# Performance work log

Measured on AMD Instinct MI355X. Metric: run time of the kernel, lower is better.

## Reference

```python
import jax, jax.numpy as jnp
import numpy as np


def setup_inputs() -> dict:
    key = jax.random.key(0)
    k1, k2, k3, k4 = jax.random.split(key, 4)
    B, C_in, C_out, H, W = 8, 256, 256, 160, 160
    mask = jax.random.randint(k1, (B, 1, H, W), 0, 2, dtype=jnp.int32)  # binary hard mask
    ori = jax.random.normal(k2, (B, C_in, H, W), dtype=jnp.float32)
    weight = jax.random.normal(k3, (C_out, C_in, 3, 3), dtype=jnp.float32) * 0.02
    bias = jax.random.normal(k4, (C_out,), dtype=jnp.float32) * 0.02
    return {"mask": mask, "ori": ori, "weight": weight, "bias": bias}


def reference(mask, ori, weight, bias):
    # apply_mask: broadcast binary [B,1,H,W] mask over channels, zero masked regions
    x = ori * mask.astype(ori.dtype)
    # dense 3x3 conv, stride 1, padding 1 (SAME) -> output [B, C_out, H, W]
    out = jax.lax.conv_general_dilated(
        x, weight,
        window_strides=(1, 1),
        padding='SAME',
        dimension_numbers=('NCHW', 'OIHW', 'NCHW'),
    )
    return out + bias[None, :, None, None]
```

## Files before the change

kernel.cpp:

```cpp
#include <hip/hip_runtime.h>

typedef __attribute__((ext_vector_type(8))) short short8;
typedef __attribute__((ext_vector_type(4))) float f32x4;

#define B_    8
#define CI    256
#define CO    256
#define Hh    160
#define Ww    160
#define HP    162
#define WP    162
#define HWp   (Hh * Ww)
#define XPAD_ELEMS (B_ * HP * WP * CI)
#define W3_ELEMS   (9 * CI * CO)
#define NT    36
#define BSLOT 8192

__device__ __forceinline__ unsigned short f2bf(float f) {
  unsigned int u = __float_as_uint(f);
  u += 0x7FFFu + ((u >> 16) & 1u);
  return (unsigned short)(u >> 16);
}

__global__ void prep_w_kernel(const float* __restrict__ w, unsigned short* __restrict__ w3) {
  int i = blockIdx.x * 256 + threadIdx.x;
  if (i >= W3_ELEMS) return;
  int e = i & 7, l = (i >> 3) & 63, g = i >> 9;
  int mi = g & 1, wm = (g >> 1) & 3, kk = (g >> 3) & 1;
  int qm = (g >> 4) & 1, cic = (g >> 5) & 3, shift = g >> 7;
  int co = qm * 128 + wm * 32 + mi * 16 + (l & 15);
  int ci = cic * 64 + kk * 32 + (l >> 4) * 8 + e;
  w3[i] = f2bf(w[(co * 256 + ci) * 9 + shift]);
}

__global__ void zero_border(unsigned short* __restrict__ xp) {
  int g = blockIdx.x * 256 + threadIdx.x;
  int pos = g >> 5;
  int c = (g & 31) << 3;
  int n = pos / 644;
  int p = pos - n * 644;
  int y, x;
  if (p < 324) { y = (p < 162) ? 0 : 161; x = (p < 162) ? p : p - 162; }
  else { int q = p - 324; y = 1 + (q >> 1); x = (q & 1) ? 161 : 0; }
  unsigned short* d = xp + (((size_t)(n * 162 + y)) * 162 + x) * 256 + c;
  *(uint4*)d = (uint4){0u, 0u, 0u, 0u};
}

__global__ void prep_x_kernel(const float* __restrict__ ori, const int* __restrict__ mask,
                              unsigned short* __restrict__ xp) {
  int bid = blockIdx.x;
  int wt = bid % 3;
  int t1 = bid / 3;
  int cit = t1 & 3;
  int t2 = t1 >> 2;
  int h = t2 % Hh;
  int n = t2 / Hh;
  int t = threadIdx.x;

  __shared__ float tile[64][65];

  int wl = t & 63;
  int w = wt * 64 + wl;
  bool valid = (w < Ww);
  float m = 0.f;
  if (valid) m = (float)mask[(n * Hh + h) * Ww + w];
  const float* src = ori + (((size_t)(n * CI + cit * 64) * Hh + h) * Ww + w);
  int r0 = t >> 6;
#pragma unroll
  for (int k = 0; k < 16; ++k) {
    int ci_l = r0 * 16 + k;
    float v = 0.f;
    if (valid) v = src[(size_t)ci_l * HWp] * m;
    tile[ci_l][wl] = v;
  }
  __syncthreads();

  int wl2 = t >> 2;
  int wo = wt * 64 + wl2;
  if (wo < Ww) {
    int cseg = (t & 3) * 16;
    union { unsigned short u[8]; uint4 v; } p0, p1;
#pragma unroll
    for (int j = 0; j < 8; ++j) p0.u[j] = f2bf(tile[cseg + j][wl2]);
#pragma unroll
    for (int j = 0; j < 8; ++j) p1.u[j] = f2bf(tile[cseg + 8 + j][wl2]);
    unsigned short* dst = xp + ((size_t)((n * HP + h + 1) * WP) + (wo + 1)) * CI + cit * 64 + cseg;
    *(uint4*)dst = p0.v;
    *(uint4*)(dst + 8) = p1.v;
  }
}

__device__ __forceinline__ void gload16(const unsigned short* g, unsigned short* l) {
  __builtin_amdgcn_global_load_lds((const __attribute__((address_space(1))) void*)g,
                                   (__attribute__((address_space(3))) void*)l, 16, 0, 0);
}

__global__ void __launch_bounds__(256, 2)
sconv_gemm(const unsigned short* __restrict__ xp, const unsigned short* __restrict__ w3,
           const float* __restrict__ bias, float* __restrict__ out) {
  __shared__ unsigned short Bs[3][BSLOT];

  const int bid = blockIdx.x;
  const int n = bid & 7;
  const int pxt = bid >> 3;
  const int p0 = pxt * 128;

  const int t = threadIdx.x;
  const int l = t & 63;
  const int wv = t >> 6;

  const int lr = l >> 3;
  const int swz8 = ((l & 7) ^ lr) << 3;
  const int lc = l & 15, hi4 = l >> 4, lx7 = l & 7;

  unsigned boff[4];
#pragma unroll
  for (int g = 0; g < 4; ++g) {
    int p = p0 + wv * 32 + g * 8 + lr;
    int h = p / Ww;
    int w = p - h * Ww;
    boff[g] = (unsigned)((n * HP + h) * WP + w) * 256 + swz8;
  }

  f32x4 acc[2][2][8];
#pragma unroll
  for (int a = 0; a < 2; ++a)
#pragma unroll
    for (int b = 0; b < 2; ++b)
#pragma unroll
      for (int c = 0; c < 8; ++c)
        acc[a][b][c] = (f32x4){0.f, 0.f, 0.f, 0.f};

  auto STAGE = [&](int ts, unsigned short* slot) {
    int cic = (ts * 57) >> 9;
    int sh = ts - cic * 9;
    int kh = (sh * 11) >> 5;
    int kw = sh - kh * 3;
    const unsigned short* src = xp + (unsigned)(kh * WP + kw) * 256 + (cic << 6);
    unsigned short* dst = slot + wv * 2048;
#pragma unroll
    for (int g = 0; g < 4; ++g)
      gload16(src + boff[g], dst + g * 512);
  };

  auto AG = [&](int ts, short8* a) {
    int cic = (ts * 57) >> 9;
    int sh = ts - cic * 9;
    const unsigned short* p = w3 + (((unsigned)(sh * 128 + cic * 32 + wv * 2)) << 9) + (l << 3);
    a[0] = *(const short8*)(p);
    a[1] = *(const short8*)(p + 512);
    a[2] = *(const short8*)(p + 4096);
    a[3] = *(const short8*)(p + 4096 + 512);
    a[4] = *(const short8*)(p + 8192);
    a[5] = *(const short8*)(p + 8192 + 512);
    a[6] = *(const short8*)(p + 8192 + 4096);
    a[7] = *(const short8*)(p + 8192 + 4096 + 512);
  };

#define BBL4(dst, slot, kk, nb) do {                                          \
  _Pragma("unroll")                                                           \
  for (int ni = 0; ni < 4; ++ni)                                              \
    dst[ni] = *(const short8*)((slot) + (((nb) + ni) * 16 + lc) * 64 +        \
                               (((((kk) << 2) + hi4) ^ lx7) << 3));           \
} while (0)

#define CL16(A, kk, bb, nb) do {                                              \
  __builtin_amdgcn_s_setprio(1);                                              \
  _Pragma("unroll")                                                           \
  for (int qm = 0; qm < 2; ++qm)                                              \
    _Pragma("unroll")                                                         \
    for (int mi = 0; mi < 2; ++mi)                                            \
      _Pragma("unroll")                                                       \
      for (int ni = 0; ni < 4; ++ni)                                          \
        acc[qm][mi][(nb) + ni] = __builtin_amdgcn_mfma_f32_16x16x32_bf16(     \
            A[qm * 4 + (kk) * 2 + mi], bb[ni], acc[qm][mi][(nb) + ni], 0, 0, 0); \
  __builtin_amdgcn_s_setprio(0);                                              \
} while (0)

  short8 aA[8], bbA[4], bbB[4];

#define TILE(tt, cur, sdst, WN) do {                                          \
  AG((tt), aA);                                    \
  if ((tt) + 2 < NT) STAGE((tt) + 2, (sdst));                                 \
  BBL4(bbA, (cur), 0, 0);                                                     \
  BBL4(bbB, (cur), 0, 4);                                                     \
  CL16(aA, 0, bbA, 0);                                                        \
  BBL4(bbA, (cur), 1, 0);                                                     \
  CL16(aA, 0, bbB, 4);                                                        \
  BBL4(bbB, (cur), 1, 4);                                                     \
  CL16(aA, 1, bbA, 0);                                                        \
  CL16(aA, 1, bbB, 4);                                                        \
  asm volatile("s_waitcnt vmcnt(" #WN ")" ::: "memory");                      \
  __builtin_amdgcn_s_barrier();                                               \
} while (0)

  unsigned short* const s0 = &Bs[0][0];
  unsigned short* const s1 = &Bs[1][0];
  unsigned short* const s2 = &Bs[2][0];

  STAGE(0, s0);
  STAGE(1, s1);
  asm volatile("s_waitcnt vmcnt(4)" ::: "memory");
  __builtin_amdgcn_s_barrier();

  for (int t3 = 0; t3 < 33; t3 += 3) {
    TILE(t3 + 0, s0, s2, 4);
    TILE(t3 + 1, s1, s0, 4);
    TILE(t3 + 2, s2, s1, 4);
  }
  TILE(33, s0, s2, 4);
  TILE(34, s1, s0, 0);
  {
    AG(35, aA);
    BBL4(bbA, s2, 0, 0);
    BBL4(bbB, s2, 0, 4);
    CL16(aA, 0, bbA, 0);
    BBL4(bbA, s2, 1, 0);
    CL16(aA, 0, bbB, 4);
    BBL4(bbB, s2, 1, 4);
    CL16(aA, 1, bbA, 0);
    CL16(aA, 1, bbB, 4);
  }

#pragma unroll
  for (int qm = 0; qm < 2; ++qm)
#pragma unroll
    for (int mi = 0; mi < 2; ++mi) {
      int cobase = qm * 128 + wv * 32 + mi * 16 + hi4 * 4;
      const float4 bv = *(const float4*)(bias + cobase);
#pragma unroll
      for (int ni = 0; ni < 8; ++ni) {
        int p = p0 + ni * 16 + lc;
        float* op = out + ((size_t)n * CO + cobase) * HWp + p;
        f32x4 v = acc[qm][mi][ni];
        op[0]               = v[0] + bv.x;
        op[(size_t)HWp]     = v[1] + bv.y;
        op[(size_t)2 * HWp] = v[2] + bv.z;
        op[(size_t)3 * HWp] = v[3] + bv.w;
      }
    }
}

extern "C" void kernel_launch(void* const* d_in, const int* in_sizes, int n_in,
                              void* d_out, int out_size, void* d_ws, size_t ws_size,
                              hipStream_t stream) {
  const int* mask = (const int*)d_in[0];
  const float* ori = (const float*)d_in[1];
  const float* weight = (const float*)d_in[2];
  const float* bias = (const float*)d_in[3];
  float* out = (float*)d_out;

  unsigned short* xp = (unsigned short*)d_ws;
  unsigned short* w3 = xp + XPAD_ELEMS;

  zero_border<<<644, 256, 0, stream>>>(xp);
  prep_w_kernel<<<(W3_ELEMS + 255) / 256, 256, 0, stream>>>(weight, w3);
  prep_x_kernel<<<B_ * Hh * 4 * 3, 256, 0, stream>>>(ori, mask, xp);
  sconv_gemm<<<1600, 256, 0, stream>>>(xp, w3, bias, out);
}
```

Before: 337.1 us.

## Retile implicit-GEMM conv to one output row per block with split-K phases

Each block now computes a full 160-pixel output row for all 256 output channels, with each wave owning 64 output channels across 10 pixel subtiles, replacing the 128-pixel by 256-channel tiles. Each tile's K step is split into four barrier-separated phases. Input staging is spread across those phases and weight fragments for the next tile are prefetched in halves. The aim is to cut per-row index math, reuse staged input across more MFMAs, and overlap global loads with compute. In exchange it uses more barriers, a larger LDS slot, 1280 blocks instead of 1600, and more accumulator registers that may lower occupancy.

```diff
diff --git a/kernel.cpp b/kernel.cpp
--- a/kernel.cpp
+++ b/kernel.cpp
@@ -14,7 +14,7 @@
 #define XPAD_ELEMS (B_ * HP * WP * CI)
 #define W3_ELEMS   (9 * CI * CO)
 #define NT    36
-#define BSLOT 8192
+#define BSLOT (160 * 64)
 
 __device__ __forceinline__ unsigned short f2bf(float f) {
   unsigned int u = __float_as_uint(f);
@@ -102,8 +102,7 @@
 
   const int bid = blockIdx.x;
   const int n = bid & 7;
-  const int pxt = bid >> 3;
-  const int p0 = pxt * 128;
+  const int h = bid >> 3;
 
   const int t = threadIdx.x;
   const int l = t & 63;
@@ -112,133 +111,131 @@
   const int lr = l >> 3;
   const int swz8 = ((l & 7) ^ lr) << 3;
   const int lc = l & 15, hi4 = l >> 4, lx7 = l & 7;
-
-  unsigned boff[4];
-#pragma unroll
-  for (int g = 0; g < 4; ++g) {
-    int p = p0 + wv * 32 + g * 8 + lr;
-    int h = p / Ww;
-    int w = p - h * Ww;
-    boff[g] = (unsigned)((n * HP + h) * WP + w) * 256 + swz8;
-  }
-
-  f32x4 acc[2][2][8];
-#pragma unroll
-  for (int a = 0; a < 2; ++a)
-#pragma unroll
-    for (int b = 0; b < 2; ++b)
-#pragma unroll
-      for (int c = 0; c < 8; ++c)
-        acc[a][b][c] = (f32x4){0.f, 0.f, 0.f, 0.f};
-
-  auto STAGE = [&](int ts, unsigned short* slot) {
-    int cic = (ts * 57) >> 9;
-    int sh = ts - cic * 9;
-    int kh = (sh * 11) >> 5;
-    int kw = sh - kh * 3;
-    const unsigned short* src = xp + (unsigned)(kh * WP + kw) * 256 + (cic << 6);
-    unsigned short* dst = slot + wv * 2048;
-#pragma unroll
-    for (int g = 0; g < 4; ++g)
-      gload16(src + boff[g], dst + g * 512);
+  const unsigned xrow = (unsigned)(n * HP + h);
+
+  unsigned boff[5];
+#pragma unroll
+  for (int k = 0; k < 5; ++k)
+    boff[k] = (unsigned)(k * 32 + wv * 8 + lr) * 256 + swz8;
+
+  f32x4 acc[4][10];
+#pragma unroll
+  for (int j = 0; j < 4; ++j)
+#pragma unroll
+    for (int ni = 0; ni < 10; ++ni)
+      acc[j][ni] = (f32x4){0.f, 0.f, 0.f, 0.f};
+
+  short8 aK0[4], aK1[4], bb[5];
+
+#define TPAR(ts, cic, sh, kh, kw)                                             \
+  const int cic = ((ts) * 57) >> 9;                                           \
+  const int sh = (ts) - cic * 9;                                              \
+  const int kh = (sh * 11) >> 5;                                              \
+  const int kw = sh - kh * 3;
+
+  auto STG = [&](int ts, unsigned short* slot, int k) {
+    TPAR(ts, cic, sh, kh, kw)
+    (void)sh;
+    const unsigned short* src = xp + ((size_t)(xrow + kh) * WP + kw) * 256 + (cic << 6) + boff[k];
+    gload16(src, slot + (k * 32 + wv * 8) * 64);
   };
 
-  auto AG = [&](int ts, short8* a) {
-    int cic = (ts * 57) >> 9;
-    int sh = ts - cic * 9;
-    const unsigned short* p = w3 + (((unsigned)(sh * 128 + cic * 32 + wv * 2)) << 9) + (l << 3);
-    a[0] = *(const short8*)(p);
-    a[1] = *(const short8*)(p + 512);
-    a[2] = *(const short8*)(p + 4096);
-    a[3] = *(const short8*)(p + 4096 + 512);
-    a[4] = *(const short8*)(p + 8192);
-    a[5] = *(const short8*)(p + 8192 + 512);
-    a[6] = *(const short8*)(p + 8192 + 4096);
-    a[7] = *(const short8*)(p + 8192 + 4096 + 512);
+  auto AGH = [&](int ts, int kk, short8* dst) {
+    TPAR(ts, cic, sh, kh, kw)
+    (void)kh; (void)kw;
+    const unsigned short* p = w3 +
+        ((size_t)(sh * 128 + cic * 32 + (wv >> 1) * 16 + ((wv & 1) << 2) + kk * 8) << 9) + (l << 3);
+#pragma unroll
+    for (int j = 0; j < 4; ++j)
+      dst[j] = *(const short8*)(p + (j << 9));
   };
 
-#define BBL4(dst, slot, kk, nb) do {                                          \
+#define BBR(slot, kk, nb) do {                                                \
   _Pragma("unroll")                                                           \
-  for (int ni = 0; ni < 4; ++ni)                                              \
-    dst[ni] = *(const short8*)((slot) + (((nb) + ni) * 16 + lc) * 64 +        \
-                               (((((kk) << 2) + hi4) ^ lx7) << 3));           \
-} while (0)
-
-#define CL16(A, kk, bb, nb) do {                                              \
+  for (int i = 0; i < 5; ++i)                                                 \
+    bb[i] = *(const short8*)((slot) + (((nb) + i) * 16 + lc) * 64 +           \
+                             (((((kk) << 2) + hi4) ^ lx7) << 3));             \
+} while (0)
+
+#define CL(AH, nb) do {                                                       \
   __builtin_amdgcn_s_setprio(1);                                              \
   _Pragma("unroll")                                                           \
-  for (int qm = 0; qm < 2; ++qm)                                              \
+  for (int j = 0; j < 4; ++j)                                                 \
     _Pragma("unroll")                                                         \
-    for (int mi = 0; mi < 2; ++mi)                                            \
-      _Pragma("unroll")                                                       \
-      for (int ni = 0; ni < 4; ++ni)                                          \
-        acc[qm][mi][(nb) + ni] = __builtin_amdgcn_mfma_f32_16x16x32_bf16(     \
-            A[qm * 4 + (kk) * 2 + mi], bb[ni], acc[qm][mi][(nb) + ni], 0, 0, 0); \
+    for (int i = 0; i < 5; ++i)                                               \
+      acc[j][(nb) + i] = __builtin_amdgcn_mfma_f32_16x16x32_bf16(             \
+          AH[j], bb[i], acc[j][(nb) + i], 0, 0, 0);                           \
   __builtin_amdgcn_s_setprio(0);                                              \
 } while (0)
 
-  short8 aA[8], bbA[4], bbB[4];
-
-#define TILE(tt, cur, sdst, WN) do {                                          \
-  AG((tt), aA);                                    \
-  if ((tt) + 2 < NT) STAGE((tt) + 2, (sdst));                                 \
-  BBL4(bbA, (cur), 0, 0);                                                     \
-  BBL4(bbB, (cur), 0, 4);                                                     \
-  CL16(aA, 0, bbA, 0);                                                        \
-  BBL4(bbA, (cur), 1, 0);                                                     \
-  CL16(aA, 0, bbB, 4);                                                        \
-  BBL4(bbB, (cur), 1, 4);                                                     \
-  CL16(aA, 1, bbA, 0);                                                        \
-  CL16(aA, 1, bbB, 4);                                                        \
-  asm volatile("s_waitcnt vmcnt(" #WN ")" ::: "memory");                      \
+#define PH(slot, kk, AH, nb, ISSUES, ENDW) do {                               \
+  ISSUES                                                                      \
+  BBR(slot, kk, nb);                                                          \
   __builtin_amdgcn_s_barrier();                                               \
+  asm volatile("s_waitcnt lgkmcnt(0)" ::: "memory");                          \
+  __builtin_amdgcn_sched_barrier(0);                                          \
+  CL(AH, nb);                                                                 \
+  ENDW                                                                        \
+  __builtin_amdgcn_s_barrier();                                               \
+} while (0)
+
+#define TILE(tt, sc, sn) do {                                                 \
+  PH(sc, 0, aK0, 0, { STG((tt) + 2, sn, 0); STG((tt) + 2, sn, 1); }, {});     \
+  PH(sc, 0, aK0, 5, { STG((tt) + 2, sn, 2); }, {});                           \
+  PH(sc, 1, aK1, 0, { AGH((tt) + 1, 0, aK0); STG((tt) + 2, sn, 3); }, {});    \
+  PH(sc, 1, aK1, 5, { STG((tt) + 2, sn, 4); },                                \
+     { AGH((tt) + 1, 1, aK1);                                                 \
+       asm volatile("s_waitcnt vmcnt(13)" ::: "memory"); });                  \
 } while (0)
 
   unsigned short* const s0 = &Bs[0][0];
   unsigned short* const s1 = &Bs[1][0];
   unsigned short* const s2 = &Bs[2][0];
 
-  STAGE(0, s0);
-  STAGE(1, s1);
-  asm volatile("s_waitcnt vmcnt(4)" ::: "memory");
+  for (int k = 0; k < 5; ++k) STG(0, s0, k);
+  for (int k = 0; k < 5; ++k) STG(1, s1, k);
+  AGH(0, 0, aK0);
+  AGH(0, 1, aK1);
+  asm volatile("s_waitcnt vmcnt(13)" ::: "memory");
   __builtin_amdgcn_s_barrier();
 
   for (int t3 = 0; t3 < 33; t3 += 3) {
-    TILE(t3 + 0, s0, s2, 4);
-    TILE(t3 + 1, s1, s0, 4);
-    TILE(t3 + 2, s2, s1, 4);
-  }
-  TILE(33, s0, s2, 4);
-  TILE(34, s1, s0, 0);
+    TILE(t3 + 0, s0, s2);
+    TILE(t3 + 1, s1, s0);
+    TILE(t3 + 2, s2, s1);
+  }
+  TILE(33, s0, s2);
+  PH(s1, 0, aK0, 0, {}, {});
+  PH(s1, 0, aK0, 5, {}, {});
+  PH(s1, 1, aK1, 0, { AGH(35, 0, aK0); }, {});
+  PH(s1, 1, aK1, 5, {},
+     { AGH(35, 1, aK1);
+       asm volatile("s_waitcnt vmcnt(8)" ::: "memory"); });
+  PH(s2, 0, aK0, 0, {}, {});
+  PH(s2, 0, aK0, 5, {}, {});
+  PH(s2, 1, aK1, 0, {}, {});
   {
-    AG(35, aA);
-    BBL4(bbA, s2, 0, 0);
-    BBL4(bbB, s2, 0, 4);
-    CL16(aA, 0, bbA, 0);
-    BBL4(bbA, s2, 1, 0);
-    CL16(aA, 0, bbB, 4);
-    BBL4(bbB, s2, 1, 4);
-    CL16(aA, 1, bbA, 0);
-    CL16(aA, 1, bbB, 4);
-  }
-
-#pragma unroll
-  for (int qm = 0; qm < 2; ++qm)
-#pragma unroll
-    for (int mi = 0; mi < 2; ++mi) {
-      int cobase = qm * 128 + wv * 32 + mi * 16 + hi4 * 4;
-      const float4 bv = *(const float4*)(bias + cobase);
-#pragma unroll
-      for (int ni = 0; ni < 8; ++ni) {
-        int p = p0 + ni * 16 + lc;
-        float* op = out + ((size_t)n * CO + cobase) * HWp + p;
-        f32x4 v = acc[qm][mi][ni];
-        op[0]               = v[0] + bv.x;
-        op[(size_t)HWp]     = v[1] + bv.y;
-        op[(size_t)2 * HWp] = v[2] + bv.z;
-        op[(size_t)3 * HWp] = v[3] + bv.w;
-      }
+    BBR(s2, 1, 5);
+    asm volatile("s_waitcnt lgkmcnt(0)" ::: "memory");
+    __builtin_amdgcn_sched_barrier(0);
+    CL(aK1, 5);
+  }
+
+#pragma unroll
+  for (int j = 0; j < 4; ++j) {
+    int cobase = wv * 64 + j * 16 + hi4 * 4;
+    const float4 bv = *(const float4*)(bias + cobase);
+    float* op = out + (((size_t)n * CO + cobase) * Hh + h) * Ww;
+#pragma unroll
+    for (int ni = 0; ni < 10; ++ni) {
+      int w = ni * 16 + lc;
+      f32x4 v = acc[j][ni];
+      op[w]                   = v[0] + bv.x;
+      op[(size_t)HWp + w]     = v[1] + bv.y;
+      op[(size_t)2 * HWp + w] = v[2] + bv.z;
+      op[(size_t)3 * HWp + w] = v[3] + bv.w;
     }
+  }
 }
 
 extern "C" void kernel_launch(void* const* d_in, const int* in_sizes, int n_in,
@@ -256,5 +253,5 @@
   zero_border<<<644, 256, 0, stream>>>(xp);
   prep_w_kernel<<<(W3_ELEMS + 255) / 256, 256, 0, stream>>>(weight, w3);
   prep_x_kernel<<<B_ * Hh * 4 * 3, 256, 0, stream>>>(ori, mask, xp);
-  sconv_gemm<<<1600, 256, 0, stream>>>(xp, w3, bias, out);
-}
+  sconv_gemm<<<1280, 256, 0, stream>>>(xp, w3, bias, out);
+}
```

After: 319.5 us. 1.06x faster.
